# Performance work log

Hardware: AMD Instinct MI355X
Metric: run time of the kernel (lower is better)

Reference implementation:

```python
import jax, jax.numpy as jnp
import numpy as np

EPS = 1e-5
H, DA, DM = 8, 64, 128  # num_read_heads, d_address, d_memory

def setup_inputs() -> dict:
    key = jax.random.key(0)
    ks = jax.random.split(key, 10)
    B, T, D, M = 4, 512, 1024, 128
    scale = lambda fan_in: 1.0 / np.sqrt(fan_in)
    return {
        "query": jax.random.normal(ks[0], (B, T, D), jnp.float32),
        "matrix": jax.random.normal(ks[1], (B, M, DA, DM), jnp.float32),
        "normalizer": jax.random.uniform(ks[2], (B, M, DA), jnp.float32),
        "addresses": jax.random.normal(ks[3], (M, DA), jnp.float32),
        "W_access": jax.random.normal(ks[4], (D, H * DA), jnp.float32) * scale(D),
        "b_access": jnp.zeros((H * DA,), jnp.float32),
        "W_read": jax.random.normal(ks[5], (D, H * DA), jnp.float32) * scale(D),
        "b_read": jnp.zeros((H * DA,), jnp.float32),
        "W_merge": jax.random.normal(ks[6], (H * DM, D), jnp.float32) * scale(H * DM),
        "b_merge": jnp.zeros((D,), jnp.float32),
    }

def reference(query, matrix, normalizer, addresses,
              W_access, b_access, W_read, b_read, W_merge, b_merge):
    act = jax.nn.softplus  # linear kernel feature map
    B, T, D = query.shape
    M = matrix.shape[1]

    # head projections -> (B,T,H,DA)
    aq = act((query @ W_access + b_access).reshape(B, T, H, DA))
    rq = act((query @ W_read + b_read).reshape(B, T, H, DA))

    # --- stage 1: linear attention over the num_memories axis ---
    ak = act(addresses)                       # (M,DA) activated keys
    norm_k = jnp.sum(ak, axis=0)              # (DA,) kernel normalizer (shared)
    den1 = jnp.einsum('btha,a->bth', aq, norm_k)[..., None] + EPS  # (B,T,H,1)

    # kernel over flattened matrix values (M, DA*DM)
    kern_m = jnp.einsum('ma,bmx->bax', ak, matrix.reshape(B, M, DA * DM))
    mat2 = jnp.einsum('btha,bax->bthx', aq, kern_m) / den1          # (B,T,H,DA*DM)
    mat2 = mat2.reshape(B, T, H, DA, DM)

    # kernel over normalizer values (M, DA)
    kern_n = jnp.einsum('ma,bmd->bad', ak, normalizer)              # (B,DA,DA)
    norm2 = jnp.einsum('btha,bad->bthd', aq, kern_n) / den1         # (B,T,H,DA)

    # --- stage 2: read from reduced kernel with read query ---
    num = jnp.einsum('btha,bthax->bthx', rq, mat2)                  # (B,T,H,DM)
    den = jnp.einsum('btha,btha->bth', rq, norm2)[..., None] + EPS
    resp = num / den                                                # (B,T,H,DM)

    return resp.reshape(B, T, H * DM) @ W_merge + b_merge           # (B,T,D)
```

## Files before the change

### kernel.cpp

```cpp
#include <hip/hip_runtime.h>
#include <hip/hip_bf16.h>
#include <math.h>

#define EPSF 1e-5f

typedef __attribute__((ext_vector_type(8))) short short8;
typedef __attribute__((ext_vector_type(4))) float f32x4;
typedef _Float16 half8 __attribute__((ext_vector_type(8)));

constexpr int Bc = 4, Tc = 512, Dc = 1024, Mc = 128, Hc = 8, DAc = 64, DMc = 128;
constexpr int BT = Bc * Tc;
constexpr int Xc = DAc * DMc;
constexpr int Rb = Tc * Hc;

__device__ __forceinline__ float softplus_f(float x) {
    return fmaxf(x, 0.f) + log1pf(expf(-fabsf(x)));
}
__device__ __forceinline__ short f2bf(float f) {
    __hip_bfloat16 h = __float2bfloat16(f);
    return *reinterpret_cast<short*>(&h);
}
__device__ __forceinline__ unsigned pk2(float a, float b) {
    return (unsigned)(unsigned short)f2bf(a) | ((unsigned)(unsigned short)f2bf(b) << 16);
}
__device__ __forceinline__ void lds_load16(void* lds, const void* g) {
    __builtin_amdgcn_global_load_lds((const __attribute__((address_space(1))) int*)g,
                                     (__attribute__((address_space(3))) int*)lds, 16, 0, 0);
}

__global__ __launch_bounds__(256) void front_kern(
        const float* __restrict__ addresses,
        const float* __restrict__ matrix,
        const float* __restrict__ normalizer,
        const float* __restrict__ query,
        const float* __restrict__ W_access,
        const float* __restrict__ W_read,
        const float* __restrict__ W_merge,
        _Float16* __restrict__ kern2,
        float* __restrict__ kern_n,
        float* __restrict__ norm_k,
        __hip_bfloat16* __restrict__ qb,
        __hip_bfloat16* __restrict__ WpT,
        __hip_bfloat16* __restrict__ WmT) {
    __shared__ float smem[8192];
    int bid = blockIdx.x;
    int tid = threadIdx.x;

    if (bid < 256) {
        float (*T)[132] = (float(*)[132])smem;
        _Float16 (*At)[40] = (_Float16(*)[40])(smem + 4224);
        int lane = tid & 63, wid = tid >> 6;
        int l15 = lane & 15, lg = lane >> 4;
        int b = bid >> 6, a = bid & 63;
        int wr = wid & 1, wc = wid >> 1;

        half8 bfrag[2][4];
#pragma unroll
        for (int cf = 0; cf < 2; cf++) {
            int a2 = wc * 32 + cf * 16 + l15;
#pragma unroll
            for (int ks = 0; ks < 4; ks++)
#pragma unroll
                for (int j = 0; j < 8; j++) {
                    int mm = ks * 32 + lg * 8 + j;
                    bfrag[cf][ks][j] = (_Float16)softplus_f(addresses[mm * 64 + a2]);
                }
        }

        const float* msrc = matrix + (size_t)b * Mc * Xc + a * DMc;
        int r = tid >> 3, ms = (tid & 7) * 16;
        int tm = tid >> 1, tk0 = (tid & 1) * 16;

        f32x4 acc[4][2];
#pragma unroll
        for (int i = 0; i < 4; i++)
#pragma unroll
            for (int j = 0; j < 2; j++) acc[i][j] = (f32x4){0.f, 0.f, 0.f, 0.f};

        float4 ld[4];
#pragma unroll
        for (int j = 0; j < 4; j++)
            ld[j] = *(const float4*)(msrc + (size_t)r * Xc + ms + j * 4);

        for (int s = 0; s < 4; s++) {
#pragma unroll
            for (int j = 0; j < 4; j++) *(float4*)&T[r][ms + j * 4] = ld[j];
            __syncthreads();
            if (s < 3) {
#pragma unroll
                for (int j = 0; j < 4; j++)
                    ld[j] = *(const float4*)(msrc + (size_t)((s + 1) * 32 + r) * Xc + ms + j * 4);
            }
            {
                half8 lo, hi;
#pragma unroll
                for (int j = 0; j < 8; j++) lo[j] = (_Float16)T[tk0 + j][tm];
#pragma unroll
                for (int j = 0; j < 8; j++) hi[j] = (_Float16)T[tk0 + 8 + j][tm];
                *(half8*)&At[tm][tk0] = lo;
                *(half8*)&At[tm][tk0 + 8] = hi;
            }
            __syncthreads();
#pragma unroll
            for (int rf = 0; rf < 4; rf++) {
                int row = wr * 64 + rf * 16 + l15;
                half8 af = *(const half8*)&At[row][lg * 8];
#pragma unroll
                for (int cf = 0; cf < 2; cf++)
                    acc[rf][cf] = __builtin_amdgcn_mfma_f32_16x16x32_f16(
                        af, bfrag[cf][s], acc[rf][cf], 0, 0, 0);
            }
            __syncthreads();
        }
        _Float16* dst = kern2 + ((size_t)(b * 64 + a)) * Mc * DAc;
#pragma unroll
        for (int rf = 0; rf < 4; rf++)
#pragma unroll
            for (int cf = 0; cf < 2; cf++) {
                int a2 = wc * 32 + cf * 16 + l15;
#pragma unroll
                for (int i = 0; i < 4; i++) {
                    int mrow = wr * 64 + rf * 16 + lg * 4 + i;
                    dst[mrow * DAc + a2] = (_Float16)acc[rf][cf][i];
                }
            }
        return;
    }
    if (bid < 288) {
        int idx = bid - 256;
        int b = idx >> 3, ch = idx & 7;
        for (int i = tid; i < Mc * DAc; i += 256) smem[i] = softplus_f(addresses[i]);
        __syncthreads();
        int d = tid & 63;
        int g = tid >> 6;
        int a2b = ch * 8 + g * 2;
        float acc0 = 0.f, acc1 = 0.f;
        const float* np = normalizer + (size_t)b * Mc * DAc + d;
        for (int mm = 0; mm < Mc; mm++) {
            float v = np[(size_t)mm * DAc];
            acc0 = fmaf(smem[mm * DAc + a2b + 0], v, acc0);
            acc1 = fmaf(smem[mm * DAc + a2b + 1], v, acc1);
        }
        kern_n[((size_t)b * DAc + a2b + 0) * DAc + d] = acc0;
        kern_n[((size_t)b * DAc + a2b + 1) * DAc + d] = acc1;
        return;
    }
    if (bid == 288) {
        for (int i = tid; i < Mc * DAc; i += 256) smem[i] = softplus_f(addresses[i]);
        __syncthreads();
        if (tid < DAc) {
            float s = 0.f;
            for (int mm = 0; mm < Mc; mm++) s += smem[mm * DAc + tid];
            norm_k[tid] = s;
        }
        return;
    }
    if (bid < 2337) {
        int i = ((bid - 289) * 256 + tid) * 4;
        float4 v = *(const float4*)(query + i);
        unsigned* d = (unsigned*)(qb + i);
        d[0] = pk2(v.x, v.y);
        d[1] = pk2(v.z, v.w);
        return;
    }
    float (*tile)[65] = (float(*)[65])smem;
    const float* S; int stride, nb, n0, kt;
    __hip_bfloat16* dst;
    if (bid < 2593) {
        int idx = bid - 2337;
        kt = idx & 15;
        n0 = (idx >> 4) * 64;
        if (n0 < 512) { S = W_access; nb = n0; }
        else          { S = W_read;   nb = n0 - 512; }
        stride = 512;
        dst = WpT;
    } else {
        int idx = bid - 2593;
        kt = idx & 15;
        n0 = (idx >> 4) * 64;
        S = W_merge; nb = n0; stride = 1024;
        dst = WmT;
    }
    {
        int kl = tid >> 2, q = tid & 3;
        const float* src = S + (size_t)(kt * 64 + kl) * stride + nb + q * 16;
#pragma unroll
        for (int j = 0; j < 4; j++) {
            float4 v = *(const float4*)(src + j * 4);
            tile[kl][q * 16 + j * 4 + 0] = v.x;
            tile[kl][q * 16 + j * 4 + 1] = v.y;
            tile[kl][q * 16 + j * 4 + 2] = v.z;
            tile[kl][q * 16 + j * 4 + 3] = v.w;
        }
    }
    __syncthreads();
    {
        int nl = tid >> 2, q = tid & 3;
        unsigned* d = (unsigned*)(dst + (size_t)(n0 + nl) * 1024 + kt * 64 + q * 16);
#pragma unroll
        for (int j = 0; j < 8; j++)
            d[j] = pk2(tile[q * 16 + j * 2][nl], tile[q * 16 + j * 2 + 1][nl]);
    }
}

template <bool SOFTPLUS, typename OutT>
__global__ __launch_bounds__(256) void gemm_bf16(const __hip_bfloat16* __restrict__ A,
                                                 const __hip_bfloat16* __restrict__ BT_,
                                                 const float* __restrict__ bias0,
                                                 const float* __restrict__ bias1, int N0,
                                                 OutT* __restrict__ C, int N, int K) {
    __shared__ short Ab[2][2][64 * 64];
    __shared__ short Bb[2][2][64 * 64];
    int tid = threadIdx.x, lane = tid & 63, wid = tid >> 6;
    int l15 = lane & 15, lg = lane >> 4;
    int rowblk = blockIdx.x * 64, colblk = blockIdx.y * 64;
    int wr = wid & 1, wc = wid >> 1;
    int srow = lane >> 3;
    int sk = ((lane & 7) ^ srow) * 8;

    f32x4 acc[2][2];
#pragma unroll
    for (int i = 0; i < 2; i++)
#pragma unroll
        for (int j = 0; j < 2; j++) acc[i][j] = (f32x4){0.f, 0.f, 0.f, 0.f};

    auto stage = [&](int kbase, int buf, int sub) {
#pragma unroll
        for (int j = 0; j < 2; j++) {
            int c = wid * 2 + j;
            int row = c * 8 + srow;
            lds_load16(&Ab[buf][sub][c * 512], A + (size_t)(rowblk + row) * K + kbase + sk);
            lds_load16(&Bb[buf][sub][c * 512], BT_ + (size_t)(colblk + row) * K + kbase + sk);
        }
    };
    stage(0, 0, 0);
    stage(64, 0, 1);
    int cur = 0;
    int nks = K >> 7;
    for (int ks = 0; ks < nks; ks++) {
        if (ks + 1 < nks) {
            stage((ks + 1) << 7, cur ^ 1, 0);
            stage(((ks + 1) << 7) + 64, cur ^ 1, 1);
            asm volatile("s_waitcnt vmcnt(8)" ::: "memory");
        } else {
            asm volatile("s_waitcnt vmcnt(0)" ::: "memory");
        }
        __builtin_amdgcn_sched_barrier(0);
        __builtin_amdgcn_s_barrier();
#pragma unroll
        for (int sub = 0; sub < 2; sub++) {
#pragma unroll
            for (int kh = 0; kh < 2; kh++) {
                short8 af[2], bfr[2];
#pragma unroll
                for (int rf = 0; rf < 2; rf++) {
                    int row = wr * 32 + rf * 16 + l15;
                    int ksw = (kh * 32 + lg * 8) ^ ((row & 7) << 3);
                    af[rf] = *(const short8*)&Ab[cur][sub][row * 64 + ksw];
                }
#pragma unroll
                for (int cf = 0; cf < 2; cf++) {
                    int col = wc * 32 + cf * 16 + l15;
                    int ksw = (kh * 32 + lg * 8) ^ ((col & 7) << 3);
                    bfr[cf] = *(const short8*)&Bb[cur][sub][col * 64 + ksw];
                }
#pragma unroll
                for (int rf = 0; rf < 2; rf++)
#pragma unroll
                    for (int cf = 0; cf < 2; cf++)
                        acc[rf][cf] = __builtin_amdgcn_mfma_f32_16x16x32_bf16(
                            af[rf], bfr[cf], acc[rf][cf], 0, 0, 0);
            }
        }
        __builtin_amdgcn_s_barrier();
        cur ^= 1;
    }
#pragma unroll
    for (int cf = 0; cf < 2; cf++) {
        int col = colblk + wc * 32 + cf * 16 + l15;
        float bv = (col < N0) ? bias0[col] : bias1[col - N0];
#pragma unroll
        for (int rf = 0; rf < 2; rf++) {
            int rbase = rowblk + wr * 32 + rf * 16 + lg * 4;
#pragma unroll
            for (int i = 0; i < 4; i++) {
                float v = acc[rf][cf][i] + bv;
                if (SOFTPLUS) v = softplus_f(v);
                C[(size_t)(rbase + i) * N + col] = (OutT)v;
            }
        }
    }
}

__global__ __launch_bounds__(256) void k4_mfma(const _Float16* __restrict__ aqrq16,
                                               const _Float16* __restrict__ kern2,
                                               const float* __restrict__ kern_n,
                                               const float* __restrict__ norm_k,
                                               __hip_bfloat16* __restrict__ resp) {
    __shared__ _Float16 Bb[2][2][64 * 64];
    __shared__ _Float16 rql[64][72];
    __shared__ float scl[64];
    __shared__ float nkl[64];
    int tid = threadIdx.x, lane = tid & 63, wid = tid >> 6;
    int l15 = lane & 15, lg = lane >> 4;
    int b = blockIdx.x >> 7;
    int rc = (blockIdx.x >> 1) & 63;
    int mh = blockIdx.x & 1;
    int rowbase = rc * 64;
    float* knl = (float*)&Bb[1][0][0];

    auto stageB = [&](int a_, int buf, int sl) {
#pragma unroll
        for (int j = 0; j < 2; j++) {
            int c = wid * 2 + j;
            int m = c * 8 + (lane >> 3);
            int sa = ((lane & 7) ^ (lane >> 3)) * 8;
            lds_load16(&Bb[buf][sl][c * 512],
                       kern2 + (((size_t)(b * 64 + a_)) * Mc + mh * 64 + m) * DAc + sa);
        }
    };
    stageB(0, 0, 0);
    stageB(1, 0, 1);
    {
#pragma unroll
        for (int j = 0; j < 4; j++) {
            int c = wid * 4 + j;
            lds_load16(knl + c * 256, kern_n + (size_t)b * 4096 + c * 256 + lane * 4);
        }
    }

    half8 aqp[4][2];
#pragma unroll
    for (int rf = 0; rf < 4; rf++)
#pragma unroll
        for (int kh = 0; kh < 2; kh++) {
            int rg = rowbase + rf * 16 + l15;
            int t_ = rg >> 3, h = rg & 7;
            aqp[rf][kh] = *(const half8*)(aqrq16 + ((size_t)(b * Tc + t_)) * 1024
                                          + h * 64 + kh * 32 + lg * 8);
        }
    {
        int row = tid >> 2, q = tid & 3;
        int rg = rowbase + row;
        int t_ = rg >> 3, h = rg & 7;
        const _Float16* src = aqrq16 + ((size_t)(b * Tc + t_)) * 1024 + 512 + h * 64 + q * 16;
        *(half8*)&rql[row][q * 16] = *(const half8*)(src);
        *(half8*)&rql[row][q * 16 + 8] = *(const half8*)(src + 8);
    }
    if (tid < 64) nkl[tid] = norm_k[tid];
    __syncthreads();

    {
        int row = wid * 16 + (lane >> 2);
        int c = lane & 3;
        int rg = rowbase + row;
        int t_ = rg >> 3, h = rg & 7;
        const _Float16* aqg = aqrq16 + ((size_t)(b * Tc + t_)) * 1024 + h * 64;
        float accj[16];
#pragma unroll
        for (int j = 0; j < 16; j++) accj[j] = 0.f;
        float d1 = 0.f;
#pragma unroll
        for (int a2c = 0; a2c < 4; a2c++) {
            half8 aa0 = *(const half8*)(aqg + a2c * 16);
            half8 aa1 = *(const half8*)(aqg + a2c * 16 + 8);
            float aqv[16];
#pragma unroll
            for (int j = 0; j < 8; j++) { aqv[j] = (float)aa0[j]; aqv[8 + j] = (float)aa1[j]; }
#pragma unroll
            for (int a2l = 0; a2l < 16; a2l++) {
                int a2 = a2c * 16 + a2l;
                float av = aqv[a2l];
                d1 = fmaf(av, nkl[a2], d1);
                const float4* kr = (const float4*)(knl + a2 * 64 + c * 16);
#pragma unroll
                for (int j4 = 0; j4 < 4; j4++) {
                    float4 kv = kr[j4];
                    accj[j4 * 4 + 0] = fmaf(av, kv.x, accj[j4 * 4 + 0]);
                    accj[j4 * 4 + 1] = fmaf(av, kv.y, accj[j4 * 4 + 1]);
                    accj[j4 * 4 + 2] = fmaf(av, kv.z, accj[j4 * 4 + 2]);
                    accj[j4 * 4 + 3] = fmaf(av, kv.w, accj[j4 * 4 + 3]);
                }
            }
        }
        float sn = 0.f;
#pragma unroll
        for (int j = 0; j < 16; j++)
            sn = fmaf((float)rql[row][c * 16 + j], accj[j], sn);
        sn += __shfl_xor(sn, 1);
        sn += __shfl_xor(sn, 2);
        if (c == 0) {
            float den1 = d1 + EPSF;
            float den = sn / den1 + EPSF;
            scl[row] = 1.f / (den1 * den);
        }
    }
    __syncthreads();

    f32x4 acc[4];
#pragma unroll
    for (int i = 0; i < 4; i++) acc[i] = (f32x4){0.f, 0.f, 0.f, 0.f};

    int mloc = wid * 16 + l15;
    int cur = 0;
    for (int it = 0; it < 32; it++) {
        if (it < 31) {
            stageB(it * 2 + 2, cur ^ 1, 0);
            stageB(it * 2 + 3, cur ^ 1, 1);
            asm volatile("s_waitcnt vmcnt(4)" ::: "memory");
        } else {
            asm volatile("s_waitcnt vmcnt(0)" ::: "memory");
        }
        __builtin_amdgcn_sched_barrier(0);
#pragma unroll
        for (int as = 0; as < 2; as++) {
            int a = it * 2 + as;
            half8 rb[4];
#pragma unroll
            for (int rf = 0; rf < 4; rf++) {
                _Float16 hv = rql[rf * 16 + l15][a];
                rb[rf] = (half8){hv, hv, hv, hv, hv, hv, hv, hv};
            }
#pragma unroll
            for (int kh = 0; kh < 2; kh++) {
                int ch = (kh * 4 + lg) ^ (mloc & 7);
                half8 bf = *(const half8*)&Bb[cur][as][mloc * 64 + ch * 8];
#pragma unroll
                for (int rf = 0; rf < 4; rf++)
                    acc[rf] = __builtin_amdgcn_mfma_f32_16x16x32_f16(
                        aqp[rf][kh] * rb[rf], bf, acc[rf], 0, 0, 0);
            }
        }
        cur ^= 1;
    }
#pragma unroll
    for (int rf = 0; rf < 4; rf++) {
#pragma unroll
        for (int i = 0; i < 4; i++) {
            int rl = rf * 16 + lg * 4 + i;
            int rg = rowbase + rl;
            float s = scl[rl];
            int t_ = rg >> 3, h = rg & 7;
            __hip_bfloat16* dst = resp + ((size_t)(b * Tc + t_)) * 1024 + h * DMc + mh * 64;
            dst[mloc] = __float2bfloat16(acc[rf][i] * s);
        }
    }
}

extern "C" void kernel_launch(void* const* d_in, const int* in_sizes, int n_in,
                              void* d_out, int out_size, void* d_ws, size_t ws_size,
                              hipStream_t stream) {
    const float* query      = (const float*)d_in[0];
    const float* matrix     = (const float*)d_in[1];
    const float* normalizer = (const float*)d_in[2];
    const float* addresses  = (const float*)d_in[3];
    const float* W_access   = (const float*)d_in[4];
    const float* b_access   = (const float*)d_in[5];
    const float* W_read     = (const float*)d_in[6];
    const float* b_read     = (const float*)d_in[7];
    const float* W_merge    = (const float*)d_in[8];
    const float* b_merge    = (const float*)d_in[9];
    float* out = (float*)d_out;
    (void)in_sizes; (void)n_in; (void)out_size; (void)ws_size;

    float* ws     = (float*)d_ws;
    float* norm_k = ws;
    float* kern_n = ws + 128;
    _Float16* aqrq16 = (_Float16*)(ws + 16512);
    _Float16* kern2  = (_Float16*)(ws + 1065088);
    __hip_bfloat16* qb   = (__hip_bfloat16*)(ws + 2113664);
    __hip_bfloat16* resp = (__hip_bfloat16*)(ws + 3162240);
    __hip_bfloat16* WpT  = (__hip_bfloat16*)(ws + 4210816);
    __hip_bfloat16* WmT  = (__hip_bfloat16*)(ws + 4735104);

    hipLaunchKernelGGL(front_kern, dim3(2849), dim3(256), 0, stream,
                       addresses, matrix, normalizer, query,
                       W_access, W_read, W_merge,
                       kern2, kern_n, norm_k, qb, WpT, WmT);
    hipLaunchKernelGGL((gemm_bf16<true, _Float16>), dim3(32, 16), dim3(256), 0, stream,
                       qb, WpT, b_access, b_read, 512, aqrq16, 1024, 1024);
    hipLaunchKernelGGL(k4_mfma, dim3(512), dim3(256), 0, stream,
                       aqrq16, kern2, kern_n, norm_k, resp);
    hipLaunchKernelGGL((gemm_bf16<false, float>), dim3(32, 16), dim3(256), 0, stream,
                       resp, WmT, b_merge, b_merge, 2048, out, 1024, 1024);
}
```

Measured before the change: 88.76 us.

## Replace double-buffered pair staging with triple-buffered single-slice pipeline in k4_mfma

The k4 main loop used to stage two address slices per iteration into a double buffer. It now uses a three-slot ring of single slices with a prefetch distance of two and issues each new load after the MFMAs that read the slot. This cuts LDS use (three slices instead of four) and spreads the global loads more evenly, which may help occupancy and latency hiding. It also moves the later prefetches after the kern_n/scale phase and its barrier. There is no barrier between finishing reads of a slot and overwriting it asynchronously, which risks a cross-wave race. The knl alias now overlaps slot 1, which is staged only after the barrier.

After: 98.70 us. +11.2%, slower.

```diff
diff --git a/kernel.cpp b/kernel.cpp
--- a/kernel.cpp
+++ b/kernel.cpp
@@ -297,7 +297,7 @@
                                                const float* __restrict__ kern_n,
                                                const float* __restrict__ norm_k,
                                                __hip_bfloat16* __restrict__ resp) {
-    __shared__ _Float16 Bb[2][2][64 * 64];
+    __shared__ _Float16 Bb[3][64 * 64];
     __shared__ _Float16 rql[64][72];
     __shared__ float scl[64];
     __shared__ float nkl[64];
@@ -307,20 +307,19 @@
     int rc = (blockIdx.x >> 1) & 63;
     int mh = blockIdx.x & 1;
     int rowbase = rc * 64;
-    float* knl = (float*)&Bb[1][0][0];
-
-    auto stageB = [&](int a_, int buf, int sl) {
+    float* knl = (float*)&Bb[1][0];
+
+    auto stageB = [&](int a_, int sl) {
 #pragma unroll
         for (int j = 0; j < 2; j++) {
             int c = wid * 2 + j;
             int m = c * 8 + (lane >> 3);
             int sa = ((lane & 7) ^ (lane >> 3)) * 8;
-            lds_load16(&Bb[buf][sl][c * 512],
+            lds_load16(&Bb[sl][c * 512],
                        kern2 + (((size_t)(b * 64 + a_)) * Mc + mh * 64 + m) * DAc + sa);
         }
     };
-    stageB(0, 0, 0);
-    stageB(1, 0, 1);
+    stageB(0, 0);
     {
 #pragma unroll
         for (int j = 0; j < 4; j++) {
@@ -397,41 +396,37 @@
     }
     __syncthreads();
 
+    stageB(1, 1);
+    stageB(2, 2);
+
     f32x4 acc[4];
 #pragma unroll
     for (int i = 0; i < 4; i++) acc[i] = (f32x4){0.f, 0.f, 0.f, 0.f};
 
     int mloc = wid * 16 + l15;
-    int cur = 0;
-    for (int it = 0; it < 32; it++) {
-        if (it < 31) {
-            stageB(it * 2 + 2, cur ^ 1, 0);
-            stageB(it * 2 + 3, cur ^ 1, 1);
-            asm volatile("s_waitcnt vmcnt(4)" ::: "memory");
-        } else {
-            asm volatile("s_waitcnt vmcnt(0)" ::: "memory");
-        }
+    int bufi = 0;
+    for (int it = 0; it < 64; it++) {
+        if (it < 62)       asm volatile("s_waitcnt vmcnt(4)" ::: "memory");
+        else if (it == 62) asm volatile("s_waitcnt vmcnt(2)" ::: "memory");
+        else               asm volatile("s_waitcnt vmcnt(0)" ::: "memory");
         __builtin_amdgcn_sched_barrier(0);
-#pragma unroll
-        for (int as = 0; as < 2; as++) {
-            int a = it * 2 + as;
-            half8 rb[4];
-#pragma unroll
-            for (int rf = 0; rf < 4; rf++) {
-                _Float16 hv = rql[rf * 16 + l15][a];
-                rb[rf] = (half8){hv, hv, hv, hv, hv, hv, hv, hv};
-            }
-#pragma unroll
-            for (int kh = 0; kh < 2; kh++) {
-                int ch = (kh * 4 + lg) ^ (mloc & 7);
-                half8 bf = *(const half8*)&Bb[cur][as][mloc * 64 + ch * 8];
-#pragma unroll
-                for (int rf = 0; rf < 4; rf++)
-                    acc[rf] = __builtin_amdgcn_mfma_f32_16x16x32_f16(
-                        aqp[rf][kh] * rb[rf], bf, acc[rf], 0, 0, 0);
-            }
-        }
-        cur ^= 1;
+        half8 rb[4];
+#pragma unroll
+        for (int rf = 0; rf < 4; rf++) {
+            _Float16 hv = rql[rf * 16 + l15][it];
+            rb[rf] = (half8){hv, hv, hv, hv, hv, hv, hv, hv};
+        }
+#pragma unroll
+        for (int kh = 0; kh < 2; kh++) {
+            int ch = (kh * 4 + lg) ^ (mloc & 7);
+            half8 bf = *(const half8*)&Bb[bufi][mloc * 64 + ch * 8];
+#pragma unroll
+            for (int rf = 0; rf < 4; rf++)
+                acc[rf] = __builtin_amdgcn_mfma_f32_16x16x32_f16(
+                    aqp[rf][kh] * rb[rf], bf, acc[rf], 0, 0, 0);
+        }
+        if (it + 3 < 64) stageB(it + 3, bufi);
+        bufi = (bufi == 2) ? 0 : bufi + 1;
     }
 #pragma unroll
     for (int rf = 0; rf < 4; rf++) {
```
